# Kernel tuning notes

Measured on AMD Instinct MI355X. Metric: run time of the kernel, lower is better.

Reference implementation:

```python
import jax, jax.numpy as jnp
import numpy as np

N_NODES = 50000
N_EDGES = 800000


def gcn_conv(x, src, dst, W, b, n):
    # PyG GCNConv: add self-loops, symmetric normalization D^-1/2 (A+I) D^-1/2,
    # linear transform, scatter-add aggregation, then bias.
    loop = jnp.arange(n, dtype=src.dtype)
    src2 = jnp.concatenate([src, loop])
    dst2 = jnp.concatenate([dst, loop])
    deg = jax.ops.segment_sum(jnp.ones(src2.shape[0], x.dtype), dst2, num_segments=n)
    dis = jnp.where(deg > 0, jax.lax.rsqrt(jnp.maximum(deg, 1e-12)), 0.0)
    norm = dis[src2] * dis[dst2]                      # [E+N]
    xw = x @ W                                        # [N, out]
    msg = xw[src2] * norm[:, None]                    # [E+N, out] gather
    out = jax.ops.segment_sum(msg, dst2, num_segments=n)  # scatter-add
    return out + b


def setup_inputs() -> dict:
    key = jax.random.key(0)
    ks = jax.random.split(key, 8)
    d_in, d_h, d_out = 128, 128, 10
    x = jax.random.normal(ks[0], (N_NODES, d_in), dtype=jnp.float32)
    edge_index = jax.random.randint(ks[1], (2, N_EDGES), 0, N_NODES, dtype=jnp.int64)
    s = 1.0 / np.sqrt(d_in)
    W1 = jax.random.normal(ks[2], (d_in, d_h), dtype=jnp.float32) * s
    b1 = jnp.zeros((d_h,), jnp.float32)
    W2 = jax.random.normal(ks[3], (d_h, d_h), dtype=jnp.float32) * s
    b2 = jnp.zeros((d_h,), jnp.float32)
    W3 = jax.random.normal(ks[4], (d_h, d_out), dtype=jnp.float32) * s
    b3 = jnp.zeros((d_out,), jnp.float32)
    return {"x": x, "edge_index": edge_index, "W1": W1, "b1": b1,
            "W2": W2, "b2": b2, "W3": W3, "b3": b3}


def reference(x, edge_index, W1, b1, W2, b2, W3, b3):
    n = x.shape[0]
    src, dst = edge_index[0], edge_index[1]
    h = gcn_conv(x, src, dst, W1, b1, n)
    h = jax.nn.relu(h)
    # dropout(p=0.5) is identity in eval mode (training=False)
    h = gcn_conv(h, src, dst, W2, b2, n)
    h = gcn_conv(h, src, dst, W3, b3, n)
    return jax.nn.log_softmax(h, axis=1)
```

## Files before the change

### kernel.cpp

```cpp
#include <hip/hip_runtime.h>
#include <cstdint>
#include <cstddef>


typedef unsigned int uint;
typedef unsigned short u16;
typedef uint  uint4e  __attribute__((ext_vector_type(4)));
typedef float float4e __attribute__((ext_vector_type(4)));
typedef uint  uint2e  __attribute__((ext_vector_type(2)));
typedef int   int2e   __attribute__((ext_vector_type(2)));
typedef int   int4e   __attribute__((ext_vector_type(4)));
using bf16x8 = __attribute__((ext_vector_type(8))) short;
using f32x4  = __attribute__((ext_vector_type(4))) float;

__device__ __forceinline__ float bf_lo(uint v) { return __uint_as_float(v << 16); }
__device__ __forceinline__ float bf_hi(uint v) { return __uint_as_float(v & 0xffff0000u); }
__device__ __forceinline__ u16 bf16_1(float a) {
    uint ua = __float_as_uint(a);
    ua = (ua + 0x7fffu + ((ua >> 16) & 1u)) >> 16;
    return (u16)ua;
}
__device__ __forceinline__ uint pack_bf2(float a, float b) {
    return (uint)bf16_1(a) | ((uint)bf16_1(b) << 16);
}

__global__ __launch_bounds__(256) void passA_wt(const int* __restrict__ ei, int E,
        int* __restrict__ cntA, int nbkt, int nca,
        const float* __restrict__ W1, const float* __restrict__ W2,
        const float* __restrict__ W3, const float* __restrict__ b2,
        u16* __restrict__ Wt1, float* __restrict__ W23, float* __restrict__ b23) {
    int tid = threadIdx.x, b = blockIdx.x;
    if (b < nca) {
        __shared__ int h[256];
        h[tid] = 0;
        __syncthreads();
        int ch = (E + nca - 1) / nca;
        int beg = b * ch, end = min(beg + ch, E);
        for (int e = beg + tid; e < end; e += 256)
            atomicAdd(&h[ei[E + e] >> 8], 1);
        __syncthreads();
        if (tid < nbkt) cntA[tid * nca + b] = h[tid];
    } else if (b == nca) {
        for (int i = 0; i < 64; ++i) {
            int idx = tid + i * 256;
            int k = idx >> 7, c = idx & 127;
            Wt1[c * 128 + k] = bf16_1(W1[idx]);
        }
        int c = tid >> 4, j0 = tid & 15;
        float acc = 0.f;
        if (c < 10) {
#pragma unroll
            for (int j = 0; j < 128; j += 16)
                acc += b2[j + j0] * W3[(j + j0) * 10 + c];
        }
#pragma unroll
        for (int m = 1; m < 16; m <<= 1) acc += __shfl_xor(acc, m);
        if (c < 10 && j0 == 0) b23[c] = acc;
    } else {
        __shared__ float w3s[1280];
        for (int i = tid; i < 1280; i += 256) w3s[i] = W3[i];
        __syncthreads();
        int idx = (b - nca - 1) * 256 + tid;
        int k = idx / 10, c = idx % 10;
        const float* w2r = W2 + (size_t)k * 128;
        float a0 = 0.f, a1 = 0.f, a2 = 0.f, a3 = 0.f;
#pragma unroll
        for (int j = 0; j < 128; j += 4) {
            a0 += w2r[j + 0] * w3s[(j + 0) * 10 + c];
            a1 += w2r[j + 1] * w3s[(j + 1) * 10 + c];
            a2 += w2r[j + 2] * w3s[(j + 2) * 10 + c];
            a3 += w2r[j + 3] * w3s[(j + 3) * 10 + c];
        }
        W23[idx] = (a0 + a1) + (a2 + a3);
    }
}

__global__ __launch_bounds__(256) void scan1(int* __restrict__ cntA, int nca,
        int* __restrict__ btot) {
    __shared__ int s[256];
    int b = blockIdx.x, tid = threadIdx.x;
    int v = cntA[b * nca + tid];
    s[tid] = v;
    __syncthreads();
    for (int d = 1; d < 256; d <<= 1) {
        int t = (tid >= d) ? s[tid - d] : 0;
        __syncthreads();
        s[tid] += t;
        __syncthreads();
    }
    cntA[b * nca + tid] = s[tid] - v;
    if (tid == 255) btot[b] = s[255];
}

__global__ __launch_bounds__(256) void scan2(const int* __restrict__ btot, int nbkt,
        int* __restrict__ bktbase, int* __restrict__ row_ptr, int n, int E) {
    __shared__ int s[256];
    int tid = threadIdx.x;
    int v = (tid < nbkt) ? btot[tid] : 0;
    s[tid] = v;
    __syncthreads();
    for (int d = 1; d < 256; d <<= 1) {
        int t = (tid >= d) ? s[tid - d] : 0;
        __syncthreads();
        s[tid] += t;
        __syncthreads();
    }
    if (tid < nbkt) bktbase[tid] = s[tid] - v;
    if (tid == 0) { bktbase[nbkt] = E; row_ptr[n] = E; }
}

__global__ __launch_bounds__(256) void passB(const int* __restrict__ ei, int E,
        const int* __restrict__ cntA, int nca, int nbkt,
        const int* __restrict__ bktbase, int2e* __restrict__ ebkt) {
    __shared__ int cur[256];
    int tid = threadIdx.x, b = blockIdx.x;
    if (tid < nbkt) cur[tid] = bktbase[tid] + cntA[tid * nca + b];
    __syncthreads();
    int ch = (E + nca - 1) / nca;
    int beg = b * ch, end = min(beg + ch, E);
    for (int e = beg + tid; e < end; e += 256) {
        int s = ei[e], d = ei[E + e];
        int pos = atomicAdd(&cur[d >> 8], 1);
        int2e pkt;
        pkt.x = s;
        pkt.y = d;
        ebkt[pos] = pkt;
    }
}

__global__ __launch_bounds__(256) void passC(const int2e* __restrict__ ebkt,
        const int* __restrict__ bktbase, int2e* __restrict__ esort,
        int* __restrict__ row_ptr, float* __restrict__ dis, int n) {
    __shared__ int fc[256];
    __shared__ int sc[256];
    int k = blockIdx.x, tid = threadIdx.x;
    int base = bktbase[k], endb = bktbase[k + 1];
    int node0 = k << 8;
    fc[tid] = 0;
    __syncthreads();
    for (int i = base + tid; i < endb; i += 256)
        atomicAdd(&fc[ebkt[i].y & 255], 1);
    __syncthreads();
    int v = fc[tid];
    sc[tid] = v;
    __syncthreads();
    for (int d = 1; d < 256; d <<= 1) {
        int t = (tid >= d) ? sc[tid - d] : 0;
        __syncthreads();
        sc[tid] += t;
        __syncthreads();
    }
    int excl = sc[tid] - v;
    if (node0 + tid < n) {
        dis[node0 + tid] = rsqrtf((float)(v + 1));
        row_ptr[node0 + tid] = base + excl;
    }
    __syncthreads();
    fc[tid] = base + excl;
    __syncthreads();
    for (int i = base + tid; i < endb; i += 256) {
        int2e ed = ebkt[i];
        int pos = atomicAdd(&fc[ed.y & 255], 1);
        esort[pos] = ed;
    }
}

__global__ __launch_bounds__(256) void normfix(int2e* __restrict__ esort,
        const float* __restrict__ dis, int E) {
    int i = blockIdx.x * blockDim.x + threadIdx.x;
    int stride = gridDim.x * blockDim.x;
    for (int e = i; e < E; e += stride) {
        int2e ed = esort[e];
        float w = dis[ed.x] * dis[ed.y];
        ed.y = __float_as_int(w);
        esort[e] = ed;
    }
}

__global__ __launch_bounds__(256) void gemm_mfma(const float* __restrict__ A,
        const u16* __restrict__ Wt, u16* __restrict__ out, int n) {
    constexpr int LDA = 136;
    __shared__ u16 as[64 * LDA];
    int tid = threadIdx.x;
    int wave = tid >> 6, lane = tid & 63;
    int row0 = blockIdx.x * 64;
    int l16 = lane & 15;
    int krow = (lane >> 4) * 8;

#pragma unroll
    for (int i = 0; i < 8; ++i) {
        int idx = tid + i * 256;
        int r = idx >> 5;
        int q = (idx & 31) * 4;
        float4e v = {0.f, 0.f, 0.f, 0.f};
        if (row0 + r < n)
            v = *reinterpret_cast<const float4e*>(A + (size_t)(row0 + r) * 128 + q);
        uint2e p;
        p.x = pack_bf2(v.x, v.y);
        p.y = pack_bf2(v.z, v.w);
        *reinterpret_cast<uint2e*>(&as[r * LDA + q]) = p;
    }

    bf16x8 b[2][4];
#pragma unroll
    for (int n2 = 0; n2 < 2; ++n2)
#pragma unroll
        for (int kb = 0; kb < 4; ++kb)
            b[n2][kb] = *reinterpret_cast<const bf16x8*>(
                Wt + (size_t)(wave * 32 + n2 * 16 + l16) * 128 + kb * 32 + krow);

    __syncthreads();

    f32x4 acc[4][2] = {};
#pragma unroll
    for (int m = 0; m < 4; ++m) {
#pragma unroll
        for (int kb = 0; kb < 4; ++kb) {
            bf16x8 a = *reinterpret_cast<const bf16x8*>(
                &as[(m * 16 + l16) * LDA + kb * 32 + krow]);
#pragma unroll
            for (int n2 = 0; n2 < 2; ++n2)
                acc[m][n2] = __builtin_amdgcn_mfma_f32_16x16x32_bf16(a, b[n2][kb], acc[m][n2], 0, 0, 0);
        }
    }

    __syncthreads();
    u16* cs = as;
#pragma unroll
    for (int m = 0; m < 4; ++m) {
        int rb = m * 16 + (lane >> 4) * 4;
#pragma unroll
        for (int n2 = 0; n2 < 2; ++n2) {
            int col = wave * 32 + n2 * 16 + l16;
#pragma unroll
            for (int r = 0; r < 4; ++r)
                cs[(rb + r) * 128 + col] = bf16_1(acc[m][n2][r]);
        }
    }
    __syncthreads();
#pragma unroll
    for (int i = 0; i < 4; ++i) {
        int idx = tid + i * 256;
        int r = idx >> 4;
        int q = (idx & 15) * 8;
        if (row0 + r < n)
            *reinterpret_cast<uint4e*>(out + (size_t)(row0 + r) * 128 + q) =
                *reinterpret_cast<const uint4e*>(&cs[r * 128 + q]);
    }
}

__device__ __forceinline__ void gather_accum(const uint* __restrict__ xw,
        const int2e* __restrict__ esort, const float* __restrict__ dis,
        int v, int lane, int beg, int end, float& ax, float& ay) {
    int e = beg;
    for (; e + 7 < end; e += 8) {
        int2e ed[8];
        uint vv[8];
#pragma unroll
        for (int j = 0; j < 8; ++j) ed[j] = esort[e + j];
#pragma unroll
        for (int j = 0; j < 8; ++j) vv[j] = xw[(size_t)ed[j].x * 64 + lane];
#pragma unroll
        for (int j = 0; j < 8; ++j) {
            float w = __int_as_float(ed[j].y);
            ax += w * bf_lo(vv[j]);
            ay += w * bf_hi(vv[j]);
        }
    }
    for (; e + 1 < end; e += 2) {
        int2e e0 = esort[e];
        int2e e1 = esort[e + 1];
        uint v0 = xw[(size_t)e0.x * 64 + lane];
        uint v1 = xw[(size_t)e1.x * 64 + lane];
        float w0 = __int_as_float(e0.y), w1 = __int_as_float(e1.y);
        ax += w0 * bf_lo(v0); ay += w0 * bf_hi(v0);
        ax += w1 * bf_lo(v1); ay += w1 * bf_hi(v1);
    }
    if (e < end) {
        int2e e0 = esort[e];
        uint v0 = xw[(size_t)e0.x * 64 + lane];
        float w0 = __int_as_float(e0.y);
        ax += w0 * bf_lo(v0); ay += w0 * bf_hi(v0);
    }
    float dv = dis[v];
    float wv = dv * dv;
    uint vs = xw[(size_t)v * 64 + lane];
    ax += wv * bf_lo(vs); ay += wv * bf_hi(vs);
}

__global__ __launch_bounds__(256) void agg_proj_kernel(const uint* __restrict__ xw,
        const int* __restrict__ row_ptr, const int2e* __restrict__ esort,
        const float* __restrict__ dis, const float* __restrict__ b1,
        const float* __restrict__ W23, float* __restrict__ z, int n) {
    int v = (int)((blockIdx.x * blockDim.x + threadIdx.x) >> 6);
    int lane = threadIdx.x & 63;
    if (v >= n) return;
    float ax = 0.f, ay = 0.f;
    gather_accum(xw, esort, dis, v, lane, row_ptr[v], row_ptr[v + 1], ax, ay);
    ax = fmaxf(ax + b1[lane * 2], 0.f);
    ay = fmaxf(ay + b1[lane * 2 + 1], 0.f);
    const float* w0 = W23 + (size_t)lane * 20;
    float p[10];
#pragma unroll
    for (int c = 0; c < 10; ++c) p[c] = ax * w0[c] + ay * w0[10 + c];
#pragma unroll
    for (int c = 0; c < 10; ++c) {
#pragma unroll
        for (int d = 1; d < 64; d <<= 1) p[c] += __shfl_xor(p[c], d);
    }
    if (lane < 10) z[(size_t)v * 10 + lane] = p[lane];
}

template <int FINAL>
__global__ __launch_bounds__(256) void agg10_kernel(const float* __restrict__ zin,
        const int* __restrict__ row_ptr, const int2e* __restrict__ esort,
        const float* __restrict__ dis, const float* __restrict__ b23,
        const float* __restrict__ b3, float* __restrict__ zout, int n) {
    int wid = (int)((blockIdx.x * blockDim.x + threadIdx.x) >> 6);
    int lane = threadIdx.x & 63;
    int grp = lane >> 4, gl = lane & 15;
    int v = wid * 4 + grp;
    bool act = (v < n);
    bool dl = (gl < 10);
    int beg = act ? row_ptr[v] : 0;
    int end = act ? row_ptr[v + 1] : 0;
    float acc = 0.f, sw = 0.f;
    int e = beg;
    for (; e + 3 < end; e += 4) {
        int2e e0 = esort[e], e1 = esort[e + 1], e2 = esort[e + 2], e3 = esort[e + 3];
        float z0 = dl ? zin[(size_t)e0.x * 10 + gl] : 0.f;
        float z1 = dl ? zin[(size_t)e1.x * 10 + gl] : 0.f;
        float z2 = dl ? zin[(size_t)e2.x * 10 + gl] : 0.f;
        float z3 = dl ? zin[(size_t)e3.x * 10 + gl] : 0.f;
        float w0 = __int_as_float(e0.y), w1 = __int_as_float(e1.y);
        float w2 = __int_as_float(e2.y), w3 = __int_as_float(e3.y);
        acc += w0 * z0 + w1 * z1 + w2 * z2 + w3 * z3;
        sw += (w0 + w1) + (w2 + w3);
    }
    for (; e < end; ++e) {
        int2e e0 = esort[e];
        float z0 = dl ? zin[(size_t)e0.x * 10 + gl] : 0.f;
        float w0 = __int_as_float(e0.y);
        acc += w0 * z0;
        sw += w0;
    }
    if (act) {
        float dv = dis[v];
        float wv = dv * dv;
        float zs = dl ? zin[(size_t)v * 10 + gl] : 0.f;
        acc += wv * zs;
        sw += wv;
    }
    if (FINAL == 0) {
        if (act && dl) zout[(size_t)v * 10 + gl] = acc;
    } else {
        float p = acc + (dl ? sw * b23[gl] + b3[gl] : 0.f);
        float m = dl ? p : -3.4e38f;
#pragma unroll
        for (int mask = 1; mask < 16; mask <<= 1) m = fmaxf(m, __shfl_xor(m, mask));
        float s = dl ? __expf(p - m) : 0.f;
#pragma unroll
        for (int mask = 1; mask < 16; mask <<= 1) s += __shfl_xor(s, mask);
        float ls = __logf(s);
        if (act && dl) zout[(size_t)v * 10 + gl] = p - m - ls;
    }
}

extern "C" void kernel_launch(void* const* d_in, const int* in_sizes, int n_in,
                              void* d_out, int out_size, void* d_ws, size_t ws_size,
                              hipStream_t stream) {
    const float* x  = (const float*)d_in[0];
    const int*   ei = (const int*)d_in[1];
    const float* W1 = (const float*)d_in[2];
    const float* b1 = (const float*)d_in[3];
    const float* W2 = (const float*)d_in[4];
    const float* b2 = (const float*)d_in[5];
    const float* W3 = (const float*)d_in[6];
    const float* b3 = (const float*)d_in[7];
    int N = in_sizes[0] / 128;
    int E = in_sizes[1] / 2;
    int NBKT = (N + 255) >> 8;
    const int NCA = 256;

    char* ws = (char*)d_ws;
    size_t off = 0;
    auto alloc = [&](size_t bytes) -> char* {
        char* p = ws + off;
        off = (off + bytes + 255) & ~(size_t)255;
        return p;
    };
    int*   cntA    = (int*)alloc((size_t)NBKT * NCA * 4);
    int*   btot    = (int*)alloc(256 * 4);
    int*   bktbase = (int*)alloc(257 * 4);
    int*   row_ptr = (int*)alloc(((size_t)N + 1) * 4);
    float* dis     = (float*)alloc((size_t)N * 4);
    u16*   Wt1     = (u16*)alloc(128 * 128 * 2);
    float* W23     = (float*)alloc(128 * 10 * 4);
    float* b23     = (float*)alloc(10 * 4);
    int2e* ebkt    = (int2e*)alloc((size_t)E * 8);
    int2e* esort   = (int2e*)alloc((size_t)E * 8);
    uint*  bufA    = (uint*)alloc((size_t)N * 64 * 4);
    float* z       = (float*)alloc((size_t)N * 10 * 4);
    float* z2      = (float*)alloc((size_t)N * 10 * 4);

    passA_wt<<<NCA + 6, 256, 0, stream>>>(ei, E, cntA, NBKT, NCA, W1, W2, W3, b2,
                                          Wt1, W23, b23);
    gemm_mfma<<<(N + 63) / 64, 256, 0, stream>>>(x, Wt1, (u16*)bufA, N);
    scan1<<<NBKT, 256, 0, stream>>>(cntA, NCA, btot);
    scan2<<<1, 256, 0, stream>>>(btot, NBKT, bktbase, row_ptr, N, E);
    passB<<<NCA, 256, 0, stream>>>(ei, E, cntA, NCA, NBKT, bktbase, ebkt);
    passC<<<NBKT, 256, 0, stream>>>(ebkt, bktbase, esort, row_ptr, dis, N);
    normfix<<<1024, 256, 0, stream>>>(esort, dis, E);
    agg_proj_kernel<<<(N + 3) / 4, 256, 0, stream>>>(bufA, row_ptr, esort, dis, b1, W23, z, N);
    agg10_kernel<0><<<(N + 15) / 16, 256, 0, stream>>>(z, row_ptr, esort, dis, nullptr, nullptr, z2, N);
    agg10_kernel<1><<<(N + 15) / 16, 256, 0, stream>>>(z2, row_ptr, esort, dis, b23, b3, (float*)d_out, N);
}
```

Measured before the change: 140.6 us.

## Fold bucket scan into passB/passC and compute edge norms on the fly

Removes the single-block scan2 kernel by having each passB and passC block redundantly prefix-sum the bucket totals in shared memory. Also drops the normfix kernel: the aggregation kernels now compute each edge weight as dis[src]*dis[dst] at gather time instead of reading a precomputed weight. This cuts two launches and a full read-modify-write pass over the sorted edge array. In exchange, every block repeats a small scan and the three aggregation kernels each do an extra random dis lookup per edge.

```diff
diff --git a/kernel.cpp b/kernel.cpp
--- a/kernel.cpp
+++ b/kernel.cpp
@@ -92,29 +92,22 @@
     if (tid == 255) btot[b] = s[255];
 }
 
-__global__ __launch_bounds__(256) void scan2(const int* __restrict__ btot, int nbkt,
-        int* __restrict__ bktbase, int* __restrict__ row_ptr, int n, int E) {
-    __shared__ int s[256];
-    int tid = threadIdx.x;
-    int v = (tid < nbkt) ? btot[tid] : 0;
-    s[tid] = v;
-    __syncthreads();
-    for (int d = 1; d < 256; d <<= 1) {
-        int t = (tid >= d) ? s[tid - d] : 0;
-        __syncthreads();
-        s[tid] += t;
-        __syncthreads();
-    }
-    if (tid < nbkt) bktbase[tid] = s[tid] - v;
-    if (tid == 0) { bktbase[nbkt] = E; row_ptr[n] = E; }
-}
-
 __global__ __launch_bounds__(256) void passB(const int* __restrict__ ei, int E,
         const int* __restrict__ cntA, int nca, int nbkt,
-        const int* __restrict__ bktbase, int2e* __restrict__ ebkt) {
+        const int* __restrict__ btot, int2e* __restrict__ ebkt) {
+    __shared__ int sc[256];
     __shared__ int cur[256];
     int tid = threadIdx.x, b = blockIdx.x;
-    if (tid < nbkt) cur[tid] = bktbase[tid] + cntA[tid * nca + b];
+    int v = (tid < nbkt) ? btot[tid] : 0;
+    sc[tid] = v;
+    __syncthreads();
+    for (int d = 1; d < 256; d <<= 1) {
+        int t = (tid >= d) ? sc[tid - d] : 0;
+        __syncthreads();
+        sc[tid] += t;
+        __syncthreads();
+    }
+    cur[tid] = (sc[tid] - v) + ((tid < nbkt) ? cntA[tid * nca + b] : 0);
     __syncthreads();
     int ch = (E + nca - 1) / nca;
     int beg = b * ch, end = min(beg + ch, E);
@@ -129,15 +122,27 @@
 }
 
 __global__ __launch_bounds__(256) void passC(const int2e* __restrict__ ebkt,
-        const int* __restrict__ bktbase, int2e* __restrict__ esort,
-        int* __restrict__ row_ptr, float* __restrict__ dis, int n) {
+        const int* __restrict__ btot, int2e* __restrict__ esort,
+        int* __restrict__ row_ptr, float* __restrict__ dis, int n, int nbkt, int E) {
+    __shared__ int sc[256];
     __shared__ int fc[256];
-    __shared__ int sc[256];
+    __shared__ int s_base;
     int k = blockIdx.x, tid = threadIdx.x;
-    int base = bktbase[k], endb = bktbase[k + 1];
+    int bt = (tid < nbkt) ? btot[tid] : 0;
+    sc[tid] = bt;
+    __syncthreads();
+    for (int d = 1; d < 256; d <<= 1) {
+        int t = (tid >= d) ? sc[tid - d] : 0;
+        __syncthreads();
+        sc[tid] += t;
+        __syncthreads();
+    }
+    if (tid == k) s_base = sc[tid] - bt;
+    fc[tid] = 0;
+    __syncthreads();
+    int base = s_base;
+    int endb = base + btot[k];
     int node0 = k << 8;
-    fc[tid] = 0;
-    __syncthreads();
     for (int i = base + tid; i < endb; i += 256)
         atomicAdd(&fc[ebkt[i].y & 255], 1);
     __syncthreads();
@@ -163,18 +168,7 @@
         int pos = atomicAdd(&fc[ed.y & 255], 1);
         esort[pos] = ed;
     }
-}
-
-__global__ __launch_bounds__(256) void normfix(int2e* __restrict__ esort,
-        const float* __restrict__ dis, int E) {
-    int i = blockIdx.x * blockDim.x + threadIdx.x;
-    int stride = gridDim.x * blockDim.x;
-    for (int e = i; e < E; e += stride) {
-        int2e ed = esort[e];
-        float w = dis[ed.x] * dis[ed.y];
-        ed.y = __float_as_int(w);
-        esort[e] = ed;
-    }
+    if (k == 0 && tid == 0) row_ptr[n] = E;
 }
 
 __global__ __launch_bounds__(256) void gemm_mfma(const float* __restrict__ A,
@@ -252,17 +246,22 @@
 __device__ __forceinline__ void gather_accum(const uint* __restrict__ xw,
         const int2e* __restrict__ esort, const float* __restrict__ dis,
         int v, int lane, int beg, int end, float& ax, float& ay) {
+    float dv = dis[v];
     int e = beg;
     for (; e + 7 < end; e += 8) {
         int2e ed[8];
         uint vv[8];
+        float wd[8];
 #pragma unroll
         for (int j = 0; j < 8; ++j) ed[j] = esort[e + j];
 #pragma unroll
-        for (int j = 0; j < 8; ++j) vv[j] = xw[(size_t)ed[j].x * 64 + lane];
-#pragma unroll
         for (int j = 0; j < 8; ++j) {
-            float w = __int_as_float(ed[j].y);
+            vv[j] = xw[(size_t)ed[j].x * 64 + lane];
+            wd[j] = dis[ed[j].x];
+        }
+#pragma unroll
+        for (int j = 0; j < 8; ++j) {
+            float w = wd[j] * dv;
             ax += w * bf_lo(vv[j]);
             ay += w * bf_hi(vv[j]);
         }
@@ -272,17 +271,16 @@
         int2e e1 = esort[e + 1];
         uint v0 = xw[(size_t)e0.x * 64 + lane];
         uint v1 = xw[(size_t)e1.x * 64 + lane];
-        float w0 = __int_as_float(e0.y), w1 = __int_as_float(e1.y);
+        float w0 = dis[e0.x] * dv, w1 = dis[e1.x] * dv;
         ax += w0 * bf_lo(v0); ay += w0 * bf_hi(v0);
         ax += w1 * bf_lo(v1); ay += w1 * bf_hi(v1);
     }
     if (e < end) {
         int2e e0 = esort[e];
         uint v0 = xw[(size_t)e0.x * 64 + lane];
-        float w0 = __int_as_float(e0.y);
+        float w0 = dis[e0.x] * dv;
         ax += w0 * bf_lo(v0); ay += w0 * bf_hi(v0);
     }
-    float dv = dis[v];
     float wv = dv * dv;
     uint vs = xw[(size_t)v * 64 + lane];
     ax += wv * bf_lo(vs); ay += wv * bf_hi(vs);
@@ -324,6 +322,7 @@
     bool dl = (gl < 10);
     int beg = act ? row_ptr[v] : 0;
     int end = act ? row_ptr[v + 1] : 0;
+    float dv = act ? dis[v] : 0.f;
     float acc = 0.f, sw = 0.f;
     int e = beg;
     for (; e + 3 < end; e += 4) {
@@ -332,20 +331,19 @@
         float z1 = dl ? zin[(size_t)e1.x * 10 + gl] : 0.f;
         float z2 = dl ? zin[(size_t)e2.x * 10 + gl] : 0.f;
         float z3 = dl ? zin[(size_t)e3.x * 10 + gl] : 0.f;
-        float w0 = __int_as_float(e0.y), w1 = __int_as_float(e1.y);
-        float w2 = __int_as_float(e2.y), w3 = __int_as_float(e3.y);
+        float w0 = dis[e0.x] * dv, w1 = dis[e1.x] * dv;
+        float w2 = dis[e2.x] * dv, w3 = dis[e3.x] * dv;
         acc += w0 * z0 + w1 * z1 + w2 * z2 + w3 * z3;
         sw += (w0 + w1) + (w2 + w3);
     }
     for (; e < end; ++e) {
         int2e e0 = esort[e];
         float z0 = dl ? zin[(size_t)e0.x * 10 + gl] : 0.f;
-        float w0 = __int_as_float(e0.y);
+        float w0 = dis[e0.x] * dv;
         acc += w0 * z0;
         sw += w0;
     }
     if (act) {
-        float dv = dis[v];
         float wv = dv * dv;
         float zs = dl ? zin[(size_t)v * 10 + gl] : 0.f;
         acc += wv * zs;
@@ -391,7 +389,6 @@
     };
     int*   cntA    = (int*)alloc((size_t)NBKT * NCA * 4);
     int*   btot    = (int*)alloc(256 * 4);
-    int*   bktbase = (int*)alloc(257 * 4);
     int*   row_ptr = (int*)alloc(((size_t)N + 1) * 4);
     float* dis     = (float*)alloc((size_t)N * 4);
     u16*   Wt1     = (u16*)alloc(128 * 128 * 2);
@@ -407,10 +404,8 @@
                                           Wt1, W23, b23);
     gemm_mfma<<<(N + 63) / 64, 256, 0, stream>>>(x, Wt1, (u16*)bufA, N);
     scan1<<<NBKT, 256, 0, stream>>>(cntA, NCA, btot);
-    scan2<<<1, 256, 0, stream>>>(btot, NBKT, bktbase, row_ptr, N, E);
-    passB<<<NCA, 256, 0, stream>>>(ei, E, cntA, NCA, NBKT, bktbase, ebkt);
-    passC<<<NBKT, 256, 0, stream>>>(ebkt, bktbase, esort, row_ptr, dis, N);
-    normfix<<<1024, 256, 0, stream>>>(esort, dis, E);
+    passB<<<NCA, 256, 0, stream>>>(ei, E, cntA, NCA, NBKT, btot, ebkt);
+    passC<<<NBKT, 256, 0, stream>>>(ebkt, btot, esort, row_ptr, dis, N, NBKT, E);
     agg_proj_kernel<<<(N + 3) / 4, 256, 0, stream>>>(bufA, row_ptr, esort, dis, b1, W23, z, N);
     agg10_kernel<0><<<(N + 15) / 16, 256, 0, stream>>>(z, row_ptr, esort, dis, nullptr, nullptr, z2, N);
     agg10_kernel<1><<<(N + 15) / 16, 256, 0, stream>>>(z2, row_ptr, esort, dis, b23, b3, (float*)d_out, N);
```

Measured after the change: 135.3 us. -3.7%, faster.
